# Performance work log

Measured on AMD Instinct MI355X. Metric: run time of the kernel, lower is better.

## Reference

```python
import jax, jax.numpy as jnp
import numpy as np

EPS = 1e-5

def _bn(x, gamma, beta):
    # BatchNorm with track_running_stats=False: batch stats over all dims but last
    axes = tuple(range(x.ndim - 1))
    mu = jnp.mean(x, axis=axes)
    var = jnp.var(x, axis=axes)  # biased, as torch uses for normalization
    return (x - mu) * jax.lax.rsqrt(var + EPS) * gamma + beta

def setup_inputs() -> dict:
    B, N, D = 8, 200, 128
    key = jax.random.key(0)
    ks = jax.random.split(key, 14)
    s = 1.0 / np.sqrt(D)
    def w(k):
        return jax.random.uniform(k, (D, D), jnp.float32, -s, s)
    def b(k):
        return jax.random.uniform(k, (D,), jnp.float32, -s, s)
    return {
        'h': jax.random.normal(ks[0], (B, N, D), jnp.float32),
        'e': jax.random.normal(ks[1], (B, N, N, D), jnp.float32),
        'Uw': w(ks[2]), 'Ub': b(ks[3]),
        'Vw': w(ks[4]), 'Vb': b(ks[5]),
        'Aw': w(ks[6]), 'Ab': b(ks[7]),
        'Bw': w(ks[8]), 'Bb': b(ks[9]),
        'Cw': w(ks[10]), 'Cb': b(ks[11]),
        'gamma_h': jnp.ones((D,), jnp.float32), 'beta_h': jnp.zeros((D,), jnp.float32),
        'gamma_e': jnp.ones((D,), jnp.float32), 'beta_e': jnp.zeros((D,), jnp.float32),
    }

def reference(h, e, Uw, Ub, Vw, Vb, Aw, Ab, Bw, Bb, Cw, Cb,
              gamma_h, beta_h, gamma_e, beta_e):
    h_in, e_in = h, e
    Uh = h @ Uw.T + Ub                      # [B,N,D]
    Vh = h @ Vw.T + Vb                      # [B,N,D]
    Ah = h @ Aw.T + Ab
    Bh = h @ Bw.T + Bb
    Ce = e @ Cw.T + Cb                      # [B,N,N,D]
    # e_new[b,i,j,d] = Ah[b,j,d] + Bh[b,i,d] + Ce[b,i,j,d]
    e_new = Ah[:, None, :, :] + Bh[:, :, None, :] + Ce
    gates = jax.nn.sigmoid(e_new)           # [B,N,N,D]
    # sum aggregation over source nodes j with Vh broadcast over i
    agg = jnp.sum(gates * Vh[:, None, :, :], axis=2)  # [B,N,D]
    h_new = Uh + agg
    h_out = h_in + jax.nn.relu(_bn(h_new, gamma_h, beta_h))
    e_out = e_in + jax.nn.relu(_bn(e_new, gamma_e, beta_e))
    return (h_out, e_out)
```

## Files before the change

kernel.cpp:

```cpp
#include <hip/hip_runtime.h>


#define B_ 8
#define N_ 200
#define D_ 128
#define BN_ (B_*N_)
#define HN_ (BN_*D_)

typedef __attribute__((ext_vector_type(8))) short short8v;
typedef __attribute__((ext_vector_type(4))) short short4v;
typedef __attribute__((ext_vector_type(4))) float float4v;
typedef __attribute__((ext_vector_type(4))) unsigned int uint4v;

__device__ __forceinline__ unsigned short f2b(float f) {
  unsigned u = __float_as_uint(f);
  u += 0x7FFFu + ((u >> 16) & 1u);
  return (unsigned short)(u >> 16);
}

__device__ __forceinline__ short8v cvt_bf16x8(float4v lo, float4v hi) {
  unsigned int r0, r1, r2, r3;
  asm("v_cvt_pk_bf16_f32 %0, %1, %2" : "=v"(r0) : "v"(lo.x), "v"(lo.y));
  asm("v_cvt_pk_bf16_f32 %0, %1, %2" : "=v"(r1) : "v"(lo.z), "v"(lo.w));
  asm("v_cvt_pk_bf16_f32 %0, %1, %2" : "=v"(r2) : "v"(hi.x), "v"(hi.y));
  asm("v_cvt_pk_bf16_f32 %0, %1, %2" : "=v"(r3) : "v"(hi.z), "v"(hi.w));
  uint4v u; u.x = r0; u.y = r1; u.z = r2; u.w = r3;
  return __builtin_bit_cast(short8v, u);
}

__global__ __launch_bounds__(256) void prelin_kernel(
    const float* __restrict__ h,
    const float* __restrict__ Uw, const float* __restrict__ Ub,
    const float* __restrict__ Vw, const float* __restrict__ Vb,
    const float* __restrict__ Aw, const float* __restrict__ Ab,
    const float* __restrict__ Bw, const float* __restrict__ Bb,
    const float* __restrict__ Cw, const float* __restrict__ Cb,
    float* __restrict__ Uh, float* __restrict__ VhT,
    float* __restrict__ AhT, float* __restrict__ BhC,
    unsigned short* __restrict__ Cwbf) {
  const int tid = threadIdx.x;
  if (blockIdx.x >= 100) {
    int g = (blockIdx.x - 100) * 1024 + tid * 4;
    float4v v = *(const float4v*)(Cw + g);
    short4v s;
    s.x = (short)f2b(v.x); s.y = (short)f2b(v.y);
    s.z = (short)f2b(v.z); s.w = (short)f2b(v.w);
    *(short4v*)(Cwbf + g) = s;
    return;
  }
  const int r0 = blockIdx.x * 16;
  __shared__ float hs[16][128];
  for (int k = 0; k < 2; k++) {
    int g = k * 256 + tid;
    int row = g >> 5, col4 = g & 31;
    *(float4v*)&hs[row][col4 * 4] =
        *(const float4v*)(h + (size_t)(r0 + row) * D_ + col4 * 4);
  }
  __syncthreads();
  const int c0 = tid, c1 = tid + 256;
  const float* w0 = (c0 < 128) ? (Uw + c0 * 128) : (Vw + (c0 - 128) * 128);
  const float  b0 = (c0 < 128) ? Ub[c0] : Vb[c0 - 128];
  const float* w1 = (c1 < 384) ? (Aw + (c1 - 256) * 128) : (Bw + (c1 - 384) * 128);
  const float  b1 = (c1 < 384) ? Ab[c1 - 256] : (Bb[c1 - 384] + Cb[c1 - 384]);
  float acc0[16], acc1[16];
#pragma unroll
  for (int r = 0; r < 16; r++) { acc0[r] = 0.f; acc1[r] = 0.f; }
  for (int k = 0; k < 128; k += 4) {
    float4v w0v = *(const float4v*)(w0 + k);
    float4v w1v = *(const float4v*)(w1 + k);
#pragma unroll
    for (int r = 0; r < 16; r++) {
      float4v hv = *(const float4v*)&hs[r][k];
      acc0[r] = fmaf(hv.x, w0v.x, fmaf(hv.y, w0v.y, fmaf(hv.z, w0v.z, fmaf(hv.w, w0v.w, acc0[r]))));
      acc1[r] = fmaf(hv.x, w1v.x, fmaf(hv.y, w1v.y, fmaf(hv.z, w1v.z, fmaf(hv.w, w1v.w, acc1[r]))));
    }
  }
  const int cc0 = c0 & 127;
  const int cc1 = (c1 - 256) & 127;
#pragma unroll
  for (int r = 0; r < 16; r++) {
    const int g = r0 + r;
    const int bb = g / 200;
    const int ii = g - bb * 200;
    float v0 = acc0[r] + b0;
    if (c0 < 128) Uh[(size_t)g * D_ + cc0] = v0;
    else          VhT[((size_t)bb * D_ + cc0) * N_ + ii] = v0;
    float v1 = acc1[r] + b1;
    if (c1 < 384) {
      AhT[((size_t)bb * D_ + cc1) * N_ + ii] = v1;
    } else {
      BhC[(size_t)g * D_ + cc1] = v1;
    }
  }
}

__global__ __launch_bounds__(256, 2) void gemm_x(
    const float* __restrict__ e, const unsigned short* __restrict__ Cwbf,
    const float* __restrict__ BhC, const float* __restrict__ AhT,
    const float* __restrict__ VhT,
    float* __restrict__ agg, float* __restrict__ psum, float* __restrict__ psumsq,
    float* __restrict__ xout) {
  const int tid = threadIdx.x;
  const int blk = blockIdx.x;
  const int b = blk / N_;
  const int lane = tid & 63, wz = tid >> 6;
  const int c = lane & 15, q = lane >> 4;

  __shared__ __align__(16) unsigned short Bs[128 * 128];

  const uint4v* bsrc = (const uint4v*)Cwbf;
#pragma unroll
  for (int k2 = 0; k2 < 8; k2++) {
    int g = k2 * 256 + tid;
    int row = g >> 4;
    int col16 = (g & 15) ^ (row & 7);
    *(uint4v*)&Bs[row * 128 + col16 * 8] = bsrc[g];
  }

  float bsev[8];
#pragma unroll
  for (int t = 0; t < 8; t++) bsev[t] = BhC[(size_t)blk * D_ + t * 16 + c];
  __syncthreads();

  const float* erow = e + (size_t)blk * N_ * D_;
  const float* AhTb = AhT + (size_t)b * D_ * N_;
  const float* VhTb = VhT + (size_t)b * D_ * N_;

  float aggv[8], sumv[8], sqv[8];
#pragma unroll
  for (int t = 0; t < 8; t++) { aggv[t] = 0.f; sumv[t] = 0.f; sqv[t] = 0.f; }

  const int sw = c & 7;

  float4v ef[8];
  {
    const int j = wz * 16 + c;
    const float* p = erow + (size_t)j * D_ + q * 8;
    const bool ok = (j < N_);
#pragma unroll
    for (int l = 0; l < 4; l++) {
      ef[2 * l]     = ok ? *(const float4v*)(p + l * 32)     : (float4v){0.f,0.f,0.f,0.f};
      ef[2 * l + 1] = ok ? *(const float4v*)(p + l * 32 + 4) : (float4v){0.f,0.f,0.f,0.f};
    }
  }

#pragma unroll
  for (int jt = 0; jt < 4; jt++) {
    const int j0 = jt * 64;
    short8v av[4];
#pragma unroll
    for (int l = 0; l < 4; l++) av[l] = cvt_bf16x8(ef[2 * l], ef[2 * l + 1]);

    if (jt < 3) {
      const int j = (jt + 1) * 64 + wz * 16 + c;
      const float* p = erow + (size_t)j * D_ + q * 8;
      const bool ok = (j < N_);
#pragma unroll
      for (int l = 0; l < 4; l++) {
        ef[2 * l]     = ok ? *(const float4v*)(p + l * 32)     : (float4v){0.f,0.f,0.f,0.f};
        ef[2 * l + 1] = ok ? *(const float4v*)(p + l * 32 + 4) : (float4v){0.f,0.f,0.f,0.f};
      }
    }

    float4v acc[8];
#pragma unroll
    for (int t = 0; t < 8; t++) acc[t] = (float4v){0.f, 0.f, 0.f, 0.f};
#pragma unroll
    for (int t = 0; t < 8; t++) {
      const unsigned short* brow = &Bs[(t * 16 + c) * 128];
#pragma unroll
      for (int l = 0; l < 4; l++) {
        short8v cw = *(const short8v*)(brow + (((q | (l << 2)) ^ sw) << 3));
        acc[t] = __builtin_amdgcn_mfma_f32_16x16x32_bf16(av[l], cw, acc[t], 0, 0, 0);
      }
    }

    const int jb = j0 + wz * 16 + q * 4;
    if (jb < N_) {
      const float* pA = AhTb + (size_t)c * N_ + jb;
      const float* pV = VhTb + (size_t)c * N_ + jb;
      float* px = xout + (size_t)blk * (N_ * D_) + (size_t)jb * D_ + c;
#pragma unroll
      for (int t = 0; t < 8; t++) {
        float4v ah4 = *(const float4v*)(pA + (size_t)t * (16 * N_));
        float4v vh4 = *(const float4v*)(pV + (size_t)t * (16 * N_));
        const float bse = bsev[t];
        float ag = aggv[t], sm = sumv[t], sq2 = sqv[t];
#pragma unroll
        for (int r = 0; r < 4; r++) {
          float x = acc[t][r] + bse + ah4[r];
          px[t * 16 + r * D_] = x;
          float g = __builtin_amdgcn_rcpf(1.0f + __expf(-x));
          ag = fmaf(g, vh4[r], ag);
          sm += x;
          sq2 = fmaf(x, x, sq2);
        }
        aggv[t] = ag; sumv[t] = sm; sqv[t] = sq2;
      }
    }
  }

  __syncthreads();
  float* red = (float*)Bs;
#pragma unroll
  for (int t = 0; t < 8; t++) {
    float a = aggv[t], s = sumv[t], sq2 = sqv[t];
    a += __shfl_xor(a, 16); a += __shfl_xor(a, 32);
    s += __shfl_xor(s, 16); s += __shfl_xor(s, 32);
    sq2 += __shfl_xor(sq2, 16); sq2 += __shfl_xor(sq2, 32);
    if (q == 0) {
      red[(0 * 4 + wz) * 128 + t * 16 + c] = a;
      red[(1 * 4 + wz) * 128 + t * 16 + c] = s;
      red[(2 * 4 + wz) * 128 + t * 16 + c] = sq2;
    }
  }
  __syncthreads();
  if (tid < 128) {
    float a = 0.f, s = 0.f, sq2 = 0.f;
#pragma unroll
    for (int w = 0; w < 4; w++) {
      a += red[(0 * 4 + w) * 128 + tid];
      s += red[(1 * 4 + w) * 128 + tid];
      sq2 += red[(2 * 4 + w) * 128 + tid];
    }
    agg[(size_t)blk * D_ + tid] = a;
    psum[(size_t)blk * D_ + tid] = s;
    psumsq[(size_t)blk * D_ + tid] = sq2;
  }
}

__global__ __launch_bounds__(256) void stats_part(
    const float* __restrict__ psum, const float* __restrict__ psumsq,
    const float* __restrict__ Uh, const float* __restrict__ agg,
    float* __restrict__ partial) {
  const int t = threadIdx.x, blk = blockIdx.x;
  const int cg = t & 31, rs = t >> 5;
  float4v ps = {0,0,0,0}, pq = {0,0,0,0}, hs = {0,0,0,0}, hq = {0,0,0,0};
#pragma unroll
  for (int p = 0; p < 2; p++) {
    const int row = blk * 16 + p * 8 + rs;
    const size_t off = (size_t)row * D_ + cg * 4;
    float4v a = *(const float4v*)(psum + off);
    float4v bq = *(const float4v*)(psumsq + off);
    float4v u = *(const float4v*)(Uh + off);
    float4v g = *(const float4v*)(agg + off);
    ps += a; pq += bq;
    float4v hv = u + g;
    hs += hv; hq += hv * hv;
  }
  __shared__ float4v red[4][8][32];
  red[0][rs][cg] = ps; red[1][rs][cg] = pq; red[2][rs][cg] = hs; red[3][rs][cg] = hq;
  __syncthreads();
  if (t < 128) {
    const int s = t >> 5, g = t & 31;
    float4v acc = red[s][0][g];
#pragma unroll
    for (int r = 1; r < 8; r++) acc += red[s][r][g];
    *(float4v*)(partial + (size_t)blk * 512 + s * 128 + g * 4) = acc;
  }
}

__global__ __launch_bounds__(256) void stats_final(
    const float* __restrict__ partial,
    const float* __restrict__ gamma_h, const float* __restrict__ beta_h,
    const float* __restrict__ gamma_e, const float* __restrict__ beta_e,
    float* __restrict__ scale_e, float* __restrict__ shift_e,
    float* __restrict__ scale_h, float* __restrict__ shift_h) {
  const int t = threadIdx.x;
  const int n = t & 127;
  if (t < 128) {
    float s = 0.f, sq = 0.f;
    for (int p = 0; p < 100; p++) {
      const float* base = partial + (size_t)p * 512;
      s += base[n]; sq += base[128 + n];
    }
    const float Me = 8.f * 200.f * 200.f;
    float mean = s / Me;
    float var = sq / Me - mean * mean;
    float sce = gamma_e[n] * rsqrtf(var + 1e-5f);
    scale_e[n] = sce; shift_e[n] = beta_e[n] - mean * sce;
  } else {
    float hs = 0.f, hq = 0.f;
    for (int p = 0; p < 100; p++) {
      const float* base = partial + (size_t)p * 512;
      hs += base[256 + n]; hq += base[384 + n];
    }
    const float Mh = (float)BN_;
    float mh = hs / Mh;
    float vh = hq / Mh - mh * mh;
    float sch = gamma_h[n] * rsqrtf(vh + 1e-5f);
    scale_h[n] = sch; shift_h[n] = beta_h[n] - mh * sch;
  }
}

__global__ __launch_bounds__(256) void fuse_out(
    const float* __restrict__ e,
    const float* __restrict__ scale_e, const float* __restrict__ shift_e,
    const float* __restrict__ hin, const float* __restrict__ Uh,
    const float* __restrict__ agg,
    const float* __restrict__ scale_h, const float* __restrict__ shift_h,
    float* __restrict__ h_out, float* __restrict__ e_out) {
  const int tid = threadIdx.x;
  const int blk = blockIdx.x;
  if (blk < 200) {
    const int idx = blk * 256 + tid;
    float4v u = ((const float4v*)Uh)[idx];
    float4v a = ((const float4v*)agg)[idx];
    float4v hv = ((const float4v*)hin)[idx];
    float4v sc = ((const float4v*)scale_h)[idx & 31];
    float4v sh = ((const float4v*)shift_h)[idx & 31];
    float4v o;
#pragma unroll
    for (int l = 0; l < 4; l++) {
      float y = fmaxf(fmaf(u[l] + a[l], sc[l], sh[l]), 0.f);
      o[l] = hv[l] + y;
    }
    ((float4v*)h_out)[idx] = o;
    return;
  }
  const size_t total8 = (size_t)BN_ * N_ * D_ / 8;
  const size_t stride = (size_t)2048 * 256;
  for (size_t i = (size_t)(blk - 200) * 256 + tid; i < total8; i += stride) {
    const size_t base = i * 8;
    const int n0 = (int)(base & 127);
    float4v x0 = *(const float4v*)(e_out + base);
    float4v x1 = *(const float4v*)(e_out + base + 4);
    float4v e0 = *(const float4v*)(e + base);
    float4v e1 = *(const float4v*)(e + base + 4);
    float4v sc0 = *(const float4v*)(scale_e + n0);
    float4v sc1 = *(const float4v*)(scale_e + n0 + 4);
    float4v sh0 = *(const float4v*)(shift_e + n0);
    float4v sh1 = *(const float4v*)(shift_e + n0 + 4);
    float4v o0, o1;
#pragma unroll
    for (int l = 0; l < 4; l++) {
      o0[l] = e0[l] + fmaxf(fmaf(x0[l], sc0[l], sh0[l]), 0.f);
      o1[l] = e1[l] + fmaxf(fmaf(x1[l], sc1[l], sh1[l]), 0.f);
    }
    *(float4v*)(e_out + base) = o0;
    *(float4v*)(e_out + base + 4) = o1;
  }
}

extern "C" void kernel_launch(void* const* d_in, const int* in_sizes, int n_in,
                              void* d_out, int out_size, void* d_ws, size_t ws_size,
                              hipStream_t stream) {
  const float* h  = (const float*)d_in[0];
  const float* e  = (const float*)d_in[1];
  const float* Uw = (const float*)d_in[2];  const float* Ub = (const float*)d_in[3];
  const float* Vw = (const float*)d_in[4];  const float* Vb = (const float*)d_in[5];
  const float* Aw = (const float*)d_in[6];  const float* Ab = (const float*)d_in[7];
  const float* Bw = (const float*)d_in[8];  const float* Bb = (const float*)d_in[9];
  const float* Cw = (const float*)d_in[10]; const float* Cb = (const float*)d_in[11];
  const float* gamma_h = (const float*)d_in[12]; const float* beta_h = (const float*)d_in[13];
  const float* gamma_e = (const float*)d_in[14]; const float* beta_e = (const float*)d_in[15];

  float* ws = (float*)d_ws;
  float* Uh   = ws + 0;
  float* VhT  = ws + (size_t)HN_;
  float* AhT  = ws + (size_t)HN_ * 2;
  float* BhC  = ws + (size_t)HN_ * 3;
  float* agg  = ws + (size_t)HN_ * 4;
  float* psum = ws + (size_t)HN_ * 5;
  float* psumsq = ws + (size_t)HN_ * 6;
  float* scale_e = ws + (size_t)HN_ * 7;
  float* shift_e = scale_e + 128;
  float* scale_h = scale_e + 256;
  float* shift_h = scale_e + 384;
  unsigned short* Cwbf = (unsigned short*)(scale_e + 512);
  float* partial = scale_e + 512 + 8192;

  float* h_out = (float*)d_out;
  float* e_out = (float*)d_out + HN_;

  prelin_kernel<<<116, 256, 0, stream>>>(h, Uw, Ub, Vw, Vb, Aw, Ab, Bw, Bb, Cw, Cb,
                                         Uh, VhT, AhT, BhC, Cwbf);
  gemm_x<<<BN_, 256, 0, stream>>>(e, Cwbf, BhC, AhT, VhT,
                                  agg, psum, psumsq, e_out);
  stats_part<<<100, 256, 0, stream>>>(psum, psumsq, Uh, agg, partial);
  stats_final<<<1, 256, 0, stream>>>(partial, gamma_h, beta_h, gamma_e, beta_e,
                                     scale_e, shift_e, scale_h, shift_h);
  fuse_out<<<2248, 256, 0, stream>>>(e, scale_e, shift_e, h, Uh, agg,
                                     scale_h, shift_h, h_out, e_out);
}
```

Measured before the change: 474.1 us.

## Split gemm_x output channels across two blocks and shrink prelin row tiles

The edge GEMM kernel now gives each (b,i) row to two blocks, each computing 64 of the 128 output channels. This halves the LDS weight tile and the accumulator registers, and the occupancy hint rises from 2 to 4 blocks per CU. The prelinear kernel now uses 4 rows per block instead of 16, which gives 400 blocks instead of 100 and more parallelism in that small stage. The cost is that each e row (200x128 floats) is read and converted to bf16 twice, once per channel half, which roughly doubles the e read traffic in gemm_x.

```diff
diff --git a/kernel.cpp b/kernel.cpp
--- a/kernel.cpp
+++ b/kernel.cpp
@@ -39,8 +39,8 @@
     float* __restrict__ AhT, float* __restrict__ BhC,
     unsigned short* __restrict__ Cwbf) {
   const int tid = threadIdx.x;
-  if (blockIdx.x >= 100) {
-    int g = (blockIdx.x - 100) * 1024 + tid * 4;
+  if (blockIdx.x >= 400) {
+    int g = (blockIdx.x - 400) * 1024 + tid * 4;
     float4v v = *(const float4v*)(Cw + g);
     short4v s;
     s.x = (short)f2b(v.x); s.y = (short)f2b(v.y);
@@ -48,11 +48,10 @@
     *(short4v*)(Cwbf + g) = s;
     return;
   }
-  const int r0 = blockIdx.x * 16;
-  __shared__ float hs[16][128];
-  for (int k = 0; k < 2; k++) {
-    int g = k * 256 + tid;
-    int row = g >> 5, col4 = g & 31;
+  const int r0 = blockIdx.x * 4;
+  __shared__ float hs[4][128];
+  if (tid < 128) {
+    int row = tid >> 5, col4 = tid & 31;
     *(float4v*)&hs[row][col4 * 4] =
         *(const float4v*)(h + (size_t)(r0 + row) * D_ + col4 * 4);
   }
@@ -62,14 +61,14 @@
   const float  b0 = (c0 < 128) ? Ub[c0] : Vb[c0 - 128];
   const float* w1 = (c1 < 384) ? (Aw + (c1 - 256) * 128) : (Bw + (c1 - 384) * 128);
   const float  b1 = (c1 < 384) ? Ab[c1 - 256] : (Bb[c1 - 384] + Cb[c1 - 384]);
-  float acc0[16], acc1[16];
-#pragma unroll
-  for (int r = 0; r < 16; r++) { acc0[r] = 0.f; acc1[r] = 0.f; }
+  float acc0[4], acc1[4];
+#pragma unroll
+  for (int r = 0; r < 4; r++) { acc0[r] = 0.f; acc1[r] = 0.f; }
   for (int k = 0; k < 128; k += 4) {
     float4v w0v = *(const float4v*)(w0 + k);
     float4v w1v = *(const float4v*)(w1 + k);
 #pragma unroll
-    for (int r = 0; r < 16; r++) {
+    for (int r = 0; r < 4; r++) {
       float4v hv = *(const float4v*)&hs[r][k];
       acc0[r] = fmaf(hv.x, w0v.x, fmaf(hv.y, w0v.y, fmaf(hv.z, w0v.z, fmaf(hv.w, w0v.w, acc0[r]))));
       acc1[r] = fmaf(hv.x, w1v.x, fmaf(hv.y, w1v.y, fmaf(hv.z, w1v.z, fmaf(hv.w, w1v.w, acc1[r]))));
@@ -78,7 +77,7 @@
   const int cc0 = c0 & 127;
   const int cc1 = (c1 - 256) & 127;
 #pragma unroll
-  for (int r = 0; r < 16; r++) {
+  for (int r = 0; r < 4; r++) {
     const int g = r0 + r;
     const int bb = g / 200;
     const int ii = g - bb * 200;
@@ -94,41 +93,42 @@
   }
 }
 
-__global__ __launch_bounds__(256, 2) void gemm_x(
+__global__ __launch_bounds__(256, 4) void gemm_x(
     const float* __restrict__ e, const unsigned short* __restrict__ Cwbf,
     const float* __restrict__ BhC, const float* __restrict__ AhT,
     const float* __restrict__ VhT,
     float* __restrict__ agg, float* __restrict__ psum, float* __restrict__ psumsq,
     float* __restrict__ xout) {
   const int tid = threadIdx.x;
-  const int blk = blockIdx.x;
-  const int b = blk / N_;
+  const int pr = blockIdx.x >> 1;
+  const int nh = blockIdx.x & 1;
+  const int b = pr / N_;
   const int lane = tid & 63, wz = tid >> 6;
   const int c = lane & 15, q = lane >> 4;
 
-  __shared__ __align__(16) unsigned short Bs[128 * 128];
+  __shared__ __align__(16) unsigned short Bs[64 * 128];
 
   const uint4v* bsrc = (const uint4v*)Cwbf;
 #pragma unroll
-  for (int k2 = 0; k2 < 8; k2++) {
+  for (int k2 = 0; k2 < 4; k2++) {
     int g = k2 * 256 + tid;
     int row = g >> 4;
     int col16 = (g & 15) ^ (row & 7);
-    *(uint4v*)&Bs[row * 128 + col16 * 8] = bsrc[g];
-  }
-
-  float bsev[8];
-#pragma unroll
-  for (int t = 0; t < 8; t++) bsev[t] = BhC[(size_t)blk * D_ + t * 16 + c];
-  __syncthreads();
-
-  const float* erow = e + (size_t)blk * N_ * D_;
-  const float* AhTb = AhT + (size_t)b * D_ * N_;
-  const float* VhTb = VhT + (size_t)b * D_ * N_;
-
-  float aggv[8], sumv[8], sqv[8];
-#pragma unroll
-  for (int t = 0; t < 8; t++) { aggv[t] = 0.f; sumv[t] = 0.f; sqv[t] = 0.f; }
+    *(uint4v*)&Bs[row * 128 + col16 * 8] = bsrc[(size_t)(nh * 64 + row) * 16 + (g & 15)];
+  }
+
+  float bsev[4];
+#pragma unroll
+  for (int t = 0; t < 4; t++) bsev[t] = BhC[(size_t)pr * D_ + nh * 64 + t * 16 + c];
+  __syncthreads();
+
+  const float* erow = e + (size_t)pr * N_ * D_;
+  const float* AhTb = AhT + (size_t)b * D_ * N_ + (size_t)(nh * 64 + c) * N_;
+  const float* VhTb = VhT + (size_t)b * D_ * N_ + (size_t)(nh * 64 + c) * N_;
+
+  float aggv[4], sumv[4], sqv[4];
+#pragma unroll
+  for (int t = 0; t < 4; t++) { aggv[t] = 0.f; sumv[t] = 0.f; sqv[t] = 0.f; }
 
   const int sw = c & 7;
 
@@ -162,11 +162,11 @@
       }
     }
 
-    float4v acc[8];
-#pragma unroll
-    for (int t = 0; t < 8; t++) acc[t] = (float4v){0.f, 0.f, 0.f, 0.f};
-#pragma unroll
-    for (int t = 0; t < 8; t++) {
+    float4v acc[4];
+#pragma unroll
+    for (int t = 0; t < 4; t++) acc[t] = (float4v){0.f, 0.f, 0.f, 0.f};
+#pragma unroll
+    for (int t = 0; t < 4; t++) {
       const unsigned short* brow = &Bs[(t * 16 + c) * 128];
 #pragma unroll
       for (int l = 0; l < 4; l++) {
@@ -177,11 +177,11 @@
 
     const int jb = j0 + wz * 16 + q * 4;
     if (jb < N_) {
-      const float* pA = AhTb + (size_t)c * N_ + jb;
-      const float* pV = VhTb + (size_t)c * N_ + jb;
-      float* px = xout + (size_t)blk * (N_ * D_) + (size_t)jb * D_ + c;
-#pragma unroll
-      for (int t = 0; t < 8; t++) {
+      const float* pA = AhTb + jb;
+      const float* pV = VhTb + jb;
+      float* px = xout + (size_t)pr * (N_ * D_) + (size_t)jb * D_ + nh * 64 + c;
+#pragma unroll
+      for (int t = 0; t < 4; t++) {
         float4v ah4 = *(const float4v*)(pA + (size_t)t * (16 * N_));
         float4v vh4 = *(const float4v*)(pV + (size_t)t * (16 * N_));
         const float bse = bsev[t];
@@ -203,29 +203,30 @@
   __syncthreads();
   float* red = (float*)Bs;
 #pragma unroll
-  for (int t = 0; t < 8; t++) {
+  for (int t = 0; t < 4; t++) {
     float a = aggv[t], s = sumv[t], sq2 = sqv[t];
     a += __shfl_xor(a, 16); a += __shfl_xor(a, 32);
     s += __shfl_xor(s, 16); s += __shfl_xor(s, 32);
     sq2 += __shfl_xor(sq2, 16); sq2 += __shfl_xor(sq2, 32);
     if (q == 0) {
-      red[(0 * 4 + wz) * 128 + t * 16 + c] = a;
-      red[(1 * 4 + wz) * 128 + t * 16 + c] = s;
-      red[(2 * 4 + wz) * 128 + t * 16 + c] = sq2;
-    }
-  }
-  __syncthreads();
-  if (tid < 128) {
+      red[(0 * 4 + wz) * 64 + t * 16 + c] = a;
+      red[(1 * 4 + wz) * 64 + t * 16 + c] = s;
+      red[(2 * 4 + wz) * 64 + t * 16 + c] = sq2;
+    }
+  }
+  __syncthreads();
+  if (tid < 64) {
     float a = 0.f, s = 0.f, sq2 = 0.f;
 #pragma unroll
     for (int w = 0; w < 4; w++) {
-      a += red[(0 * 4 + w) * 128 + tid];
-      s += red[(1 * 4 + w) * 128 + tid];
-      sq2 += red[(2 * 4 + w) * 128 + tid];
-    }
-    agg[(size_t)blk * D_ + tid] = a;
-    psum[(size_t)blk * D_ + tid] = s;
-    psumsq[(size_t)blk * D_ + tid] = sq2;
+      a += red[(0 * 4 + w) * 64 + tid];
+      s += red[(1 * 4 + w) * 64 + tid];
+      sq2 += red[(2 * 4 + w) * 64 + tid];
+    }
+    const size_t o = (size_t)pr * D_ + nh * 64 + tid;
+    agg[o] = a;
+    psum[o] = s;
+    psumsq[o] = sq2;
   }
 }
 
@@ -373,10 +374,10 @@
   float* h_out = (float*)d_out;
   float* e_out = (float*)d_out + HN_;
 
-  prelin_kernel<<<116, 256, 0, stream>>>(h, Uw, Ub, Vw, Vb, Aw, Ab, Bw, Bb, Cw, Cb,
+  prelin_kernel<<<416, 256, 0, stream>>>(h, Uw, Ub, Vw, Vb, Aw, Ab, Bw, Bb, Cw, Cb,
                                          Uh, VhT, AhT, BhC, Cwbf);
-  gemm_x<<<BN_, 256, 0, stream>>>(e, Cwbf, BhC, AhT, VhT,
-                                  agg, psum, psumsq, e_out);
+  gemm_x<<<BN_ * 2, 256, 0, stream>>>(e, Cwbf, BhC, AhT, VhT,
+                                      agg, psum, psumsq, e_out);
   stats_part<<<100, 256, 0, stream>>>(psum, psumsq, Uh, agg, partial);
   stats_final<<<1, 256, 0, stream>>>(partial, gamma_h, beta_h, gamma_e, beta_e,
                                      scale_e, shift_e, scale_h, shift_h);
```

Result: slower. 572.4 us (+20.7%).

## Split gemm_x over j halves to double grid and hoist e loads

Applied to the files above, without the earlier changes.

Each (b,i) row's j range is split across two blocks, giving 3200 blocks with 2 j-tiles each instead of 1600 blocks with 4. Partial agg, sum and sumsq are written per half and combined in stats_part and fuse_out. The first e tile and the bias loads are issued before the Cw shared-memory staging so they overlap it. The aim is better occupancy and latency hiding, at the cost of loading Cw into LDS twice as often, larger partial buffers, and the second half doing partly masked work (j 128-199 plus padding).

```diff
diff --git a/kernel.cpp b/kernel.cpp
--- a/kernel.cpp
+++ b/kernel.cpp
@@ -98,16 +98,34 @@
     const float* __restrict__ e, const unsigned short* __restrict__ Cwbf,
     const float* __restrict__ BhC, const float* __restrict__ AhT,
     const float* __restrict__ VhT,
-    float* __restrict__ agg, float* __restrict__ psum, float* __restrict__ psumsq,
+    float* __restrict__ agg2, float* __restrict__ psum2, float* __restrict__ psumsq2,
     float* __restrict__ xout) {
   const int tid = threadIdx.x;
-  const int blk = blockIdx.x;
-  const int b = blk / N_;
+  const int pr = blockIdx.x >> 1;
+  const int jh = blockIdx.x & 1;
+  const int b = pr / N_;
   const int lane = tid & 63, wz = tid >> 6;
   const int c = lane & 15, q = lane >> 4;
+  const int jbase = jh * 128;
+
+  const float* erow = e + (size_t)pr * N_ * D_;
+
+  float4v ef[8];
+  {
+    const int j = jbase + wz * 16 + c;
+    const float* p = erow + (size_t)j * D_ + q * 8;
+    const bool ok = (j < N_);
+#pragma unroll
+    for (int l = 0; l < 4; l++) {
+      ef[2 * l]     = ok ? *(const float4v*)(p + l * 32)     : (float4v){0.f,0.f,0.f,0.f};
+      ef[2 * l + 1] = ok ? *(const float4v*)(p + l * 32 + 4) : (float4v){0.f,0.f,0.f,0.f};
+    }
+  }
+  float bsev[8];
+#pragma unroll
+  for (int t = 0; t < 8; t++) bsev[t] = BhC[(size_t)pr * D_ + t * 16 + c];
 
   __shared__ __align__(16) unsigned short Bs[128 * 128];
-
   const uint4v* bsrc = (const uint4v*)Cwbf;
 #pragma unroll
   for (int k2 = 0; k2 < 8; k2++) {
@@ -116,13 +134,8 @@
     int col16 = (g & 15) ^ (row & 7);
     *(uint4v*)&Bs[row * 128 + col16 * 8] = bsrc[g];
   }
-
-  float bsev[8];
-#pragma unroll
-  for (int t = 0; t < 8; t++) bsev[t] = BhC[(size_t)blk * D_ + t * 16 + c];
-  __syncthreads();
-
-  const float* erow = e + (size_t)blk * N_ * D_;
+  __syncthreads();
+
   const float* AhTb = AhT + (size_t)b * D_ * N_;
   const float* VhTb = VhT + (size_t)b * D_ * N_;
 
@@ -132,27 +145,14 @@
 
   const int sw = c & 7;
 
-  float4v ef[8];
-  {
-    const int j = wz * 16 + c;
-    const float* p = erow + (size_t)j * D_ + q * 8;
-    const bool ok = (j < N_);
-#pragma unroll
-    for (int l = 0; l < 4; l++) {
-      ef[2 * l]     = ok ? *(const float4v*)(p + l * 32)     : (float4v){0.f,0.f,0.f,0.f};
-      ef[2 * l + 1] = ok ? *(const float4v*)(p + l * 32 + 4) : (float4v){0.f,0.f,0.f,0.f};
-    }
-  }
-
-#pragma unroll
-  for (int jt = 0; jt < 4; jt++) {
-    const int j0 = jt * 64;
+#pragma unroll
+  for (int jtl = 0; jtl < 2; jtl++) {
     short8v av[4];
 #pragma unroll
     for (int l = 0; l < 4; l++) av[l] = cvt_bf16x8(ef[2 * l], ef[2 * l + 1]);
 
-    if (jt < 3) {
-      const int j = (jt + 1) * 64 + wz * 16 + c;
+    if (jtl < 1) {
+      const int j = jbase + 64 + wz * 16 + c;
       const float* p = erow + (size_t)j * D_ + q * 8;
       const bool ok = (j < N_);
 #pragma unroll
@@ -175,11 +175,11 @@
       }
     }
 
-    const int jb = j0 + wz * 16 + q * 4;
+    const int jb = jbase + jtl * 64 + wz * 16 + q * 4;
     if (jb < N_) {
       const float* pA = AhTb + (size_t)c * N_ + jb;
       const float* pV = VhTb + (size_t)c * N_ + jb;
-      float* px = xout + (size_t)blk * (N_ * D_) + (size_t)jb * D_ + c;
+      float* px = xout + (size_t)pr * (N_ * D_) + (size_t)jb * D_ + c;
 #pragma unroll
       for (int t = 0; t < 8; t++) {
         float4v ah4 = *(const float4v*)(pA + (size_t)t * (16 * N_));
@@ -223,15 +223,16 @@
       s += red[(1 * 4 + w) * 128 + tid];
       sq2 += red[(2 * 4 + w) * 128 + tid];
     }
-    agg[(size_t)blk * D_ + tid] = a;
-    psum[(size_t)blk * D_ + tid] = s;
-    psumsq[(size_t)blk * D_ + tid] = sq2;
+    const size_t o = (size_t)pr * 256 + jh * 128 + tid;
+    agg2[o] = a;
+    psum2[o] = s;
+    psumsq2[o] = sq2;
   }
 }
 
 __global__ __launch_bounds__(256) void stats_part(
-    const float* __restrict__ psum, const float* __restrict__ psumsq,
-    const float* __restrict__ Uh, const float* __restrict__ agg,
+    const float* __restrict__ psum2, const float* __restrict__ psumsq2,
+    const float* __restrict__ Uh, const float* __restrict__ agg2,
     float* __restrict__ partial) {
   const int t = threadIdx.x, blk = blockIdx.x;
   const int cg = t & 31, rs = t >> 5;
@@ -239,13 +240,16 @@
 #pragma unroll
   for (int p = 0; p < 2; p++) {
     const int row = blk * 16 + p * 8 + rs;
-    const size_t off = (size_t)row * D_ + cg * 4;
-    float4v a = *(const float4v*)(psum + off);
-    float4v bq = *(const float4v*)(psumsq + off);
-    float4v u = *(const float4v*)(Uh + off);
-    float4v g = *(const float4v*)(agg + off);
-    ps += a; pq += bq;
-    float4v hv = u + g;
+    const size_t b2 = (size_t)row * 256 + cg * 4;
+    float4v a0 = *(const float4v*)(psum2 + b2);
+    float4v a1 = *(const float4v*)(psum2 + b2 + 128);
+    float4v q0 = *(const float4v*)(psumsq2 + b2);
+    float4v q1 = *(const float4v*)(psumsq2 + b2 + 128);
+    float4v g0 = *(const float4v*)(agg2 + b2);
+    float4v g1 = *(const float4v*)(agg2 + b2 + 128);
+    float4v u = *(const float4v*)(Uh + (size_t)row * D_ + cg * 4);
+    ps += a0 + a1; pq += q0 + q1;
+    float4v hv = u + g0 + g1;
     hs += hv; hq += hv * hv;
   }
   __shared__ float4v red[4][8][32];
@@ -297,18 +301,20 @@
     const float* __restrict__ e,
     const float* __restrict__ scale_e, const float* __restrict__ shift_e,
     const float* __restrict__ hin, const float* __restrict__ Uh,
-    const float* __restrict__ agg,
+    const float* __restrict__ agg2,
     const float* __restrict__ scale_h, const float* __restrict__ shift_h,
     float* __restrict__ h_out, float* __restrict__ e_out) {
   const int tid = threadIdx.x;
   const int blk = blockIdx.x;
   if (blk < 200) {
     const int idx = blk * 256 + tid;
+    const int pr = idx >> 5, sl = idx & 31;
+    const float4v* ag = (const float4v*)agg2;
+    float4v a = ag[(size_t)pr * 64 + sl] + ag[(size_t)pr * 64 + 32 + sl];
     float4v u = ((const float4v*)Uh)[idx];
-    float4v a = ((const float4v*)agg)[idx];
     float4v hv = ((const float4v*)hin)[idx];
-    float4v sc = ((const float4v*)scale_h)[idx & 31];
-    float4v sh = ((const float4v*)shift_h)[idx & 31];
+    float4v sc = ((const float4v*)scale_h)[sl];
+    float4v sh = ((const float4v*)shift_h)[sl];
     float4v o;
 #pragma unroll
     for (int l = 0; l < 4; l++) {
@@ -356,14 +362,14 @@
   const float* gamma_e = (const float*)d_in[14]; const float* beta_e = (const float*)d_in[15];
 
   float* ws = (float*)d_ws;
-  float* Uh   = ws + 0;
-  float* VhT  = ws + (size_t)HN_;
-  float* AhT  = ws + (size_t)HN_ * 2;
-  float* BhC  = ws + (size_t)HN_ * 3;
-  float* agg  = ws + (size_t)HN_ * 4;
-  float* psum = ws + (size_t)HN_ * 5;
-  float* psumsq = ws + (size_t)HN_ * 6;
-  float* scale_e = ws + (size_t)HN_ * 7;
+  float* Uh     = ws + 0;
+  float* VhT    = ws + (size_t)HN_;
+  float* AhT    = ws + (size_t)HN_ * 2;
+  float* BhC    = ws + (size_t)HN_ * 3;
+  float* agg2   = ws + (size_t)HN_ * 4;
+  float* psum2  = ws + (size_t)HN_ * 6;
+  float* psumsq2= ws + (size_t)HN_ * 8;
+  float* scale_e = ws + (size_t)HN_ * 10;
   float* shift_e = scale_e + 128;
   float* scale_h = scale_e + 256;
   float* shift_h = scale_e + 384;
@@ -375,11 +381,11 @@
 
   prelin_kernel<<<116, 256, 0, stream>>>(h, Uw, Ub, Vw, Vb, Aw, Ab, Bw, Bb, Cw, Cb,
                                          Uh, VhT, AhT, BhC, Cwbf);
-  gemm_x<<<BN_, 256, 0, stream>>>(e, Cwbf, BhC, AhT, VhT,
-                                  agg, psum, psumsq, e_out);
-  stats_part<<<100, 256, 0, stream>>>(psum, psumsq, Uh, agg, partial);
+  gemm_x<<<BN_ * 2, 256, 0, stream>>>(e, Cwbf, BhC, AhT, VhT,
+                                      agg2, psum2, psumsq2, e_out);
+  stats_part<<<100, 256, 0, stream>>>(psum2, psumsq2, Uh, agg2, partial);
   stats_final<<<1, 256, 0, stream>>>(partial, gamma_h, beta_h, gamma_e, beta_e,
                                      scale_e, shift_e, scale_h, shift_h);
-  fuse_out<<<2248, 256, 0, stream>>>(e, scale_e, shift_e, h, Uh, agg,
+  fuse_out<<<2248, 256, 0, stream>>>(e, scale_e, shift_e, h, Uh, agg2,
                                      scale_h, shift_h, h_out, e_out);
 }
```

New measurement: 479.7 us. No clear change (+1.2%).
